# Optimization experiments

Measured on AMD Instinct MI355X. Metric: run time of the kernel, lower is better.

## Reference

```python
import jax, jax.numpy as jnp
import numpy as np
from jax import lax

# dims
B = 1024          # batch
C_IN = 8          # board feature planes
HW = 8            # board side
FN = 16           # filter_num
SEN, INT, OUT = 1024, 2048, 1024
TOT = SEN + INT + OUT            # 4096
CNN_OUT = sum((HW - k + 1) ** 2 for k in range(1, 9)) * FN  # 204*FN = 3264
NUM_OUT = 1968
LORA_R = 64
LORA_SCALE = 128.0 / LORA_R      # alpha / rank = 2.0
TIMESTEPS = 5
DENSITY = 0.3


def setup_inputs() -> dict:
    key = jax.random.key(0)
    ks = jax.random.split(key, 20)
    inp = {"x": jax.random.normal(ks[0], (B, HW, HW, C_IN), dtype=jnp.float32)}
    # conv bank: kernels 1..8, OIHW layout
    for i, k in enumerate(range(1, 9)):
        inp[f"conv_w{k}"] = jax.random.normal(ks[1 + i], (FN, C_IN, k, k), dtype=jnp.float32) * (1.0 / np.sqrt(C_IN * k * k))
    inp["conv_b"] = jnp.zeros((8, FN), dtype=jnp.float32)
    # recurrent weight with sparsity pattern (mask = W != 0, as in register_buffer('sparsity_mask', W_init != 0))
    Wd = jax.random.normal(ks[9], (TOT, TOT), dtype=jnp.float32) * 0.02
    mask = (jax.random.uniform(ks[10], (TOT, TOT)) < DENSITY).astype(jnp.float32)
    inp["W"] = Wd * mask
    inp["lora_A"] = jax.random.normal(ks[11], (TOT, LORA_R), dtype=jnp.float32) * 0.02
    inp["lora_B"] = jax.random.normal(ks[12], (LORA_R, TOT), dtype=jnp.float32) * 0.02
    inp["ip_w"] = jax.random.normal(ks[13], (CNN_OUT, SEN), dtype=jnp.float32) * (1.0 / np.sqrt(CNN_OUT))
    inp["ip_b"] = jnp.zeros((SEN,), dtype=jnp.float32)
    inp["out_w"] = jax.random.normal(ks[14], (OUT, NUM_OUT), dtype=jnp.float32) * (1.0 / np.sqrt(OUT))
    inp["out_b"] = jnp.zeros((NUM_OUT,), dtype=jnp.float32)
    return inp


def _forward(x, conv_w1, conv_w2, conv_w3, conv_w4, conv_w5, conv_w6, conv_w7, conv_w8,
             conv_b, W, lora_A, lora_B, ip_w, ip_b, out_w, out_b):
    xn = jnp.transpose(x, (0, 3, 1, 2))  # NHWC -> NCHW, as x.permute(0,3,1,2)
    feats = []
    for i, cw in enumerate([conv_w1, conv_w2, conv_w3, conv_w4, conv_w5, conv_w6, conv_w7, conv_w8]):
        y = lax.conv_general_dilated(xn, cw, (1, 1), 'VALID',
                                     dimension_numbers=('NCHW', 'OIHW', 'NCHW'))
        y = jax.nn.relu(y + conv_b[i][None, :, None, None])  # use_relu=True
        feats.append(y.reshape(y.shape[0], -1))
    feat = jnp.concatenate(feats, axis=1)  # [B, CNN_OUT]

    # effective W with LoRA + sparsity mask
    mask = (W != 0).astype(W.dtype)
    W_eff = (W + (lora_A @ lora_B) * LORA_SCALE) * mask

    E = feat @ ip_w + ip_b                           # input_proj (no dropout: drop_out=False)
    E_pad = jnp.pad(E, ((0, 0), (0, TOT - SEN)))     # E feeds only the sensory block

    # The nine block matmuls S@Wss + I@Wrs + O@Wos etc. equal slices of state @ W_eff.
    state = jnp.zeros((x.shape[0], TOT), dtype=W.dtype)
    for t in range(TIMESTEPS):
        nxt = state @ W_eff
        if t == 0:
            nxt = nxt + E_pad
        nxt = state + nxt          # use_residual=True
        state = jax.nn.relu(nxt)

    O_state = state[:, SEN + INT:]
    return O_state @ out_w + out_b


def reference(x, conv_w1, conv_w2, conv_w3, conv_w4, conv_w5, conv_w6, conv_w7, conv_w8,
              conv_b, W, lora_A, lora_B, ip_w, ip_b, out_w, out_b):
    return _forward(x, conv_w1, conv_w2, conv_w3, conv_w4, conv_w5, conv_w6, conv_w7, conv_w8,
                    conv_b, W, lora_A, lora_B, ip_w, ip_b, out_w, out_b)
```

## Files before the change

kernel.cpp:

```cpp
#include <hip/hip_runtime.h>
#include <stdint.h>

typedef unsigned short u16;
typedef __attribute__((ext_vector_type(8))) short bf16x8;
typedef __attribute__((ext_vector_type(4))) float f32x4;

__device__ __forceinline__ u16 f2bf(float f) {
  union { float f; uint32_t u; } v; v.f = f;
  uint32_t u = v.u;
  return (u16)((u + 0x7fffu + ((u >> 16) & 1u)) >> 16);
}

__device__ __forceinline__ void gl_lds16(const void* g, void* l) {
  __builtin_amdgcn_global_load_lds(
      (const __attribute__((address_space(1))) uint32_t*)g,
      (__attribute__((address_space(3))) uint32_t*)l, 16, 0, 0);
}

__constant__ int c_off[9] = {0, 1024, 1808, 2384, 2784, 3040, 3184, 3248, 3264};

__global__ __launch_bounds__(256)
void prep_all(const float* __restrict__ x, u16* __restrict__ Xb,
              const float* __restrict__ lA, u16* __restrict__ lAb,
              const float* __restrict__ ip_w, u16* __restrict__ ip_wt,
              const float* __restrict__ out_w, u16* __restrict__ out_wt,
              const float* __restrict__ lB, u16* __restrict__ lBt,
              const float* w1, const float* w2, const float* w3, const float* w4,
              const float* w5, const float* w6, const float* w7, const float* w8,
              const float* __restrict__ cb,
              u16* __restrict__ Wct, float* __restrict__ bias_c) {
  __shared__ float tile[64][65];
  int b = blockIdx.x;
  const int t = threadIdx.x;
  if (b < 512) {
    const int i = b * 256 + t;
    const float4 v = ((const float4*)x)[i];
    ((ushort4*)Xb)[i] = make_ushort4(f2bf(v.x), f2bf(v.y), f2bf(v.z), f2bf(v.w));
    return;
  }
  b -= 512;
  if (b < 256) {
    const int i = b * 256 + t;
    const float4 v = ((const float4*)lA)[i];
    ((ushort4*)lAb)[i] = make_ushort4(f2bf(v.x), f2bf(v.y), f2bf(v.z), f2bf(v.w));
    return;
  }
  b -= 256;
  if (b < 1392) {
    const float* src; u16* dst; int R, C, bx, by;
    if (b < 816)        { src = ip_w;  dst = ip_wt;  R = 3264; C = 1024; bx = b % 16; by = b / 16; }
    else if (b < 1328)  { b -= 816;  src = out_w; dst = out_wt; R = 1024; C = 1968; bx = b % 32; by = b / 32; }
    else                { b -= 1328; src = lB;    dst = lBt;    R = 64;   C = 4096; bx = b;      by = 0; }
    const int rb = by << 6, cbs = bx << 6;
    for (int i = 0; i < 16; ++i) {
      const int idx = t + (i << 8);
      const int r = idx >> 6, c = idx & 63;
      float v = 0.f;
      if (cbs + c < C) v = src[(size_t)(rb + r) * C + cbs + c];
      tile[r][c] = v;
    }
    __syncthreads();
    for (int i = 0; i < 16; ++i) {
      const int idx = t + (i << 8);
      const int c = idx >> 6, r = idx & 63;
      dst[(size_t)(cbs + c) * R + rb + r] = f2bf(tile[r][c]);
    }
    return;
  }
  const int o = b - 1392;
  u16* row = Wct + (size_t)o * 512;
  if (t < 128) *(ushort4*)(row + (t << 2)) = make_ushort4(0, 0, 0, 0);
  if (o >= 3264) {
    if (t == 0) bias_c[o] = 0.f;
    return;
  }
  __syncthreads();
  const float* ws[8] = {w1, w2, w3, w4, w5, w6, w7, w8};
  int kidx = 0;
  while (o >= c_off[kidx + 1]) ++kidx;
  const int ks = kidx + 1;
  const int s  = 8 - kidx;
  const int r  = o - c_off[kidx];
  const int f   = r / (s * s);
  const int rem = r - f * s * s;
  const int oi  = rem / s;
  const int oj  = rem - oi * s;
  const float* w = ws[kidx] + (size_t)f * 8 * ks * ks;
  const int ne = 8 * ks * ks;
  for (int e = t; e < ne; e += 256) {
    const int c  = e / (ks * ks);
    const int er = e - c * ks * ks;
    const int di = er / ks;
    const int dj = er - di * ks;
    row[((oi + di) * 8 + (oj + dj)) * 8 + c] = f2bf(w[(c * ks + di) * ks + dj]);
  }
  if (t == 0) bias_c[o] = cb[kidx * 16 + f];
}

__global__ __launch_bounds__(256)
void weff2(const float* __restrict__ W, const u16* __restrict__ lBt,
           const u16* __restrict__ lAb, u16* __restrict__ Wt) {
  __shared__ __align__(16) u16 As_[64 * 64];
  __shared__ __align__(16) u16 Bs_[64 * 64];
  __shared__ __align__(16) float Wl[64 * 64];
  __shared__ u16 Ct[64 * 68];
  const int t = threadIdx.x;
  const int w = t >> 6, lane = t & 63;
  const int nb = blockIdx.x << 6, kb = blockIdx.y << 6;
  const int m0 = (w & 1) << 5, n0 = (w >> 1) << 5;
  const int lr = lane & 15, lq = lane >> 4;

  for (int i = 0; i < 2; ++i) {
    const int c   = (w << 7) + (i << 6) + lane;
    const int row = c >> 3;
    const int kg  = (c & 7) ^ (row & 7);
    gl_lds16(lBt + (size_t)(nb + row) * 64 + (kg << 3), (char*)As_ + c * 16);
    gl_lds16(lAb + (size_t)(kb + row) * 64 + (kg << 3), (char*)Bs_ + c * 16);
  }
  for (int i = 0; i < 4; ++i) {
    const int c   = (w << 8) + (i << 6) + lane;
    const int row = c >> 4;
    const int cc  = (c & 15) ^ (row & 15);
    gl_lds16(W + (size_t)(kb + row) * 4096 + nb + (cc << 2), (char*)Wl + c * 16);
  }
  __syncthreads();

  f32x4 acc[2][2] = {};
  for (int kk = 0; kk < 2; ++kk) {
    const int kg = (kk << 2) + lq;
    const int sw = (kg ^ (lr & 7)) << 3;
    bf16x8 af[2], bf[2];
    for (int i = 0; i < 2; ++i)
      af[i] = *(const bf16x8*)&As_[(m0 + (i << 4) + lr) * 64 + sw];
    for (int j = 0; j < 2; ++j)
      bf[j] = *(const bf16x8*)&Bs_[(n0 + (j << 4) + lr) * 64 + sw];
    for (int i = 0; i < 2; ++i)
      for (int j = 0; j < 2; ++j)
        acc[i][j] = __builtin_amdgcn_mfma_f32_16x16x32_bf16(af[i], bf[j], acc[i][j], 0, 0, 0);
  }

  for (int i = 0; i < 2; ++i) {
    for (int j = 0; j < 2; ++j) {
      const int cg  = n0 + (j << 4) + lr;
      const int rg0 = m0 + (i << 4) + (lq << 2);
      const int ch  = (rg0 >> 2) ^ (cg & 15);
      const float4 wv4 = *(const float4*)&Wl[cg * 64 + (ch << 2)];
      const float wv[4] = {wv4.x, wv4.y, wv4.z, wv4.w};
      for (int r = 0; r < 4; ++r)
        Ct[(rg0 + r) * 68 + cg] =
            (wv[r] != 0.f) ? f2bf(wv[r] + 2.0f * acc[i][j][r]) : (u16)0;
    }
  }
  __syncthreads();

  const int row = t >> 2, kp = (t & 3) << 4;
  u16* dst = Wt + (size_t)(nb + row) * 4096 + kb + kp;
  const u16* src = &Ct[row * 68 + kp];
  for (int i = 0; i < 4; ++i)
    *(ushort4*)(dst + (i << 2)) = *(const ushort4*)(src + (i << 2));
}

template<int EPI, int NR>
__global__ __launch_bounds__(256)
void gemm3b(const u16* __restrict__ A, int lda,
            const u16* __restrict__ Bt, int ldb, int K,
            const float* __restrict__ bias,
            const float* __restrict__ st_in, int st_ld,
            float* __restrict__ outf, int outf_ld,
            u16* __restrict__ outb, int outb_ld, int nvalid) {
  constexpr int BN = NR * 32;
  __shared__ __align__(16) u16 As[3][64 * 64];
  __shared__ __align__(16) u16 Bs[3][BN * 64];
  const int t = threadIdx.x;
  const int w = t >> 6, lane = t & 63;
  const int mb = blockIdx.y << 6, nb = blockIdx.x * BN;
  const int m0 = (w & 1) << 5, n0 = (w >> 1) * (NR << 4);
  const int lr = lane & 15, lq = lane >> 4;

  f32x4 acc[2][NR] = {};
  const int nk = K >> 6;

  auto stage = [&](int kt, int buf) {
    const int kb = kt << 6;
#pragma unroll
    for (int i = 0; i < 2; ++i) {
      const int c   = (w << 7) + (i << 6) + lane;
      const int row = c >> 3;
      const int kg  = (c & 7) ^ (row & 7);
      gl_lds16(A + (size_t)(mb + row) * lda + kb + (kg << 3),
               (char*)As[buf] + c * 16);
    }
#pragma unroll
    for (int i = 0; i < NR; ++i) {
      const int c   = w * (NR * 64) + (i << 6) + lane;
      const int row = c >> 3;
      const int kg  = (c & 7) ^ (row & 7);
      gl_lds16(Bt + (size_t)(nb + row) * ldb + kb + (kg << 3),
               (char*)Bs[buf] + c * 16);
    }
  };

  stage(0, 0);
  stage(1, 1);
  for (int kt = 0; kt < nk; ++kt) {
    const int buf = kt % 3;
    if (kt + 1 < nk) {
      if constexpr (NR == 4) asm volatile("s_waitcnt vmcnt(6)" ::: "memory");
      else                   asm volatile("s_waitcnt vmcnt(4)" ::: "memory");
    } else {
      asm volatile("s_waitcnt vmcnt(0)" ::: "memory");
    }
    __builtin_amdgcn_s_barrier();
    asm volatile("" ::: "memory");
    __builtin_amdgcn_sched_barrier(0);
    if (kt + 2 < nk) stage(kt + 2, (kt + 2) % 3);
    __builtin_amdgcn_s_setprio(1);
#pragma unroll
    for (int kk = 0; kk < 2; ++kk) {
      const int kg = (kk << 2) + lq;
      const int sw = (kg ^ (lr & 7)) << 3;
      bf16x8 af[2], bf[NR];
#pragma unroll
      for (int i = 0; i < 2; ++i)
        af[i] = *(const bf16x8*)&As[buf][(m0 + (i << 4) + lr) * 64 + sw];
#pragma unroll
      for (int j = 0; j < NR; ++j)
        bf[j] = *(const bf16x8*)&Bs[buf][(n0 + (j << 4) + lr) * 64 + sw];
#pragma unroll
      for (int i = 0; i < 2; ++i)
#pragma unroll
        for (int j = 0; j < NR; ++j)
          acc[i][j] = __builtin_amdgcn_mfma_f32_16x16x32_bf16(af[i], bf[j], acc[i][j], 0, 0, 0);
    }
    __builtin_amdgcn_s_setprio(0);
  }

#pragma unroll
  for (int i = 0; i < 2; ++i) {
#pragma unroll
    for (int j = 0; j < NR; ++j) {
      const int cg = nb + n0 + (j << 4) + lr;
#pragma unroll
      for (int r = 0; r < 4; ++r) {
        const int rg = mb + m0 + (i << 4) + (lq << 2) + r;
        float v = acc[i][j][r];
        if (EPI == 1) {
          v += st_in[(size_t)rg * st_ld + cg];
          v = v > 0.f ? v : 0.f;
          outf[(size_t)rg * outf_ld + cg] = v;
          outb[(size_t)rg * outb_ld + cg] = f2bf(v);
        } else if (EPI == 2) {
          if (cg < nvalid)
            outf[(size_t)rg * outf_ld + cg] = v + bias[cg];
        } else {
          v += bias[cg];
          v = v > 0.f ? v : 0.f;
          outb[(size_t)rg * outb_ld + cg] = f2bf(v);
        }
      }
    }
  }
}

__global__ __launch_bounds__(256)
void gemm_e3b(const u16* __restrict__ A, const u16* __restrict__ Bt,
              float* __restrict__ part) {
  __shared__ __align__(16) u16 As[3][64 * 64];
  __shared__ __align__(16) u16 Bs[3][128 * 64];
  const int t = threadIdx.x;
  const int w = t >> 6, lane = t & 63;
  const int mb = blockIdx.y << 6, nb = blockIdx.x << 7;
  const int m0 = (w & 1) << 5, n0 = (w >> 1) << 6;
  const int lr = lane & 15, lq = lane >> 4;
  const int z = blockIdx.z;
  const int k0 = z * 832;
  const int nk = (z == 3) ? 12 : 13;

  f32x4 acc[2][4] = {};

  auto stage = [&](int kt, int buf) {
    const int kb = k0 + (kt << 6);
#pragma unroll
    for (int i = 0; i < 2; ++i) {
      const int c   = (w << 7) + (i << 6) + lane;
      const int row = c >> 3;
      const int kg  = (c & 7) ^ (row & 7);
      gl_lds16(A + (size_t)(mb + row) * 3328 + kb + (kg << 3),
               (char*)As[buf] + c * 16);
    }
#pragma unroll
    for (int i = 0; i < 4; ++i) {
      const int c   = (w << 8) + (i << 6) + lane;
      const int row = c >> 3;
      const int kg  = (c & 7) ^ (row & 7);
      gl_lds16(Bt + (size_t)(nb + row) * 3264 + kb + (kg << 3),
               (char*)Bs[buf] + c * 16);
    }
  };

  stage(0, 0);
  stage(1, 1);
  for (int kt = 0; kt < nk; ++kt) {
    const int buf = kt % 3;
    if (kt + 1 < nk) asm volatile("s_waitcnt vmcnt(6)" ::: "memory");
    else             asm volatile("s_waitcnt vmcnt(0)" ::: "memory");
    __builtin_amdgcn_s_barrier();
    asm volatile("" ::: "memory");
    __builtin_amdgcn_sched_barrier(0);
    if (kt + 2 < nk) stage(kt + 2, (kt + 2) % 3);
    __builtin_amdgcn_s_setprio(1);
#pragma unroll
    for (int kk = 0; kk < 2; ++kk) {
      const int kg = (kk << 2) + lq;
      const int sw = (kg ^ (lr & 7)) << 3;
      bf16x8 af[2], bf[4];
#pragma unroll
      for (int i = 0; i < 2; ++i)
        af[i] = *(const bf16x8*)&As[buf][(m0 + (i << 4) + lr) * 64 + sw];
#pragma unroll
      for (int j = 0; j < 4; ++j)
        bf[j] = *(const bf16x8*)&Bs[buf][(n0 + (j << 4) + lr) * 64 + sw];
#pragma unroll
      for (int i = 0; i < 2; ++i)
#pragma unroll
        for (int j = 0; j < 4; ++j)
          acc[i][j] = __builtin_amdgcn_mfma_f32_16x16x32_bf16(af[i], bf[j], acc[i][j], 0, 0, 0);
    }
    __builtin_amdgcn_s_setprio(0);
  }

  float* dst = part + (size_t)z * 1024 * 1024;
#pragma unroll
  for (int i = 0; i < 2; ++i)
#pragma unroll
    for (int j = 0; j < 4; ++j) {
      const int cg = nb + n0 + (j << 4) + lr;
#pragma unroll
      for (int r = 0; r < 4; ++r) {
        const int rg = mb + m0 + (i << 4) + (lq << 2) + r;
        dst[(size_t)rg * 1024 + cg] = acc[i][j][r];
      }
    }
}

__global__ __launch_bounds__(256)
void e_combine(const float* __restrict__ part, const float* __restrict__ bias,
               float* __restrict__ st_f, u16* __restrict__ st_b) {
  const int i = (blockIdx.x * 256 + threadIdx.x) << 2;
  const int row = i >> 12, col = i & 4095;
  if (col < 1024) {
    const int pi = (row << 10) + col;
    const float4 a = *(const float4*)&part[pi];
    const float4 b = *(const float4*)&part[1024 * 1024 + pi];
    const float4 c = *(const float4*)&part[2 * 1024 * 1024 + pi];
    const float4 d = *(const float4*)&part[3 * 1024 * 1024 + pi];
    const float4 bs = *(const float4*)&bias[col];
    float v[4] = {a.x + b.x + c.x + d.x + bs.x, a.y + b.y + c.y + d.y + bs.y,
                  a.z + b.z + c.z + d.z + bs.z, a.w + b.w + c.w + d.w + bs.w};
    u16 o[4];
    for (int r = 0; r < 4; ++r) {
      v[r] = v[r] > 0.f ? v[r] : 0.f;
      o[r] = f2bf(v[r]);
    }
    *(float4*)&st_f[i] = make_float4(v[0], v[1], v[2], v[3]);
    *(ushort4*)&st_b[i] = make_ushort4(o[0], o[1], o[2], o[3]);
  } else {
    *(float4*)&st_f[i] = make_float4(0.f, 0.f, 0.f, 0.f);
    *(ushort4*)&st_b[i] = make_ushort4(0, 0, 0, 0);
  }
}

extern "C" void kernel_launch(void* const* d_in, const int* in_sizes, int n_in,
                              void* d_out, int out_size, void* d_ws, size_t ws_size,
                              hipStream_t stream) {
  const float* x     = (const float*)d_in[0];
  const float* cw[8];
  for (int i = 0; i < 8; ++i) cw[i] = (const float*)d_in[1 + i];
  const float* convb = (const float*)d_in[9];
  const float* W     = (const float*)d_in[10];
  const float* lA    = (const float*)d_in[11];
  const float* lB    = (const float*)d_in[12];
  const float* ip_w  = (const float*)d_in[13];
  const float* ip_b  = (const float*)d_in[14];
  const float* out_w = (const float*)d_in[15];
  const float* out_b = (const float*)d_in[16];
  float* out = (float*)d_out;

  char* p = (char*)d_ws;
  u16* feat   = (u16*)p;  p += (size_t)1024 * 3328 * 2;
  u16* ip_wt  = (u16*)p;  p += (size_t)1024 * 3264 * 2;
  u16* out_wt = (u16*)p;  p += (size_t)2048 * 1024 * 2;
  u16* Wt     = (u16*)p;  p += (size_t)4096 * 4096 * 2;
  float* st_f[2];
  st_f[0] = (float*)p;    p += (size_t)1024 * 4096 * 4;
  st_f[1] = (float*)p;    p += (size_t)1024 * 4096 * 4;
  u16* st_b[2];
  st_b[0] = (u16*)p;      p += (size_t)1024 * 4096 * 2;
  st_b[1] = (u16*)p;      p += (size_t)1024 * 4096 * 2;

  char* q = (char*)st_f[1];
  u16* Xb       = (u16*)q;  q += (size_t)1024 * 512 * 2;
  u16* Wct      = (u16*)q;  q += (size_t)3328 * 512 * 2;
  float* bias_c = (float*)q; q += (size_t)3328 * 4;
  u16* lBt      = (u16*)q;  q += (size_t)4096 * 64 * 2;
  u16* lAb      = (u16*)q;  q += (size_t)4096 * 64 * 2;
  float* Epart  = (float*)st_f[1];

  prep_all<<<5488, 256, 0, stream>>>(x, Xb, lA, lAb, ip_w, ip_wt,
                                     out_w, out_wt, lB, lBt,
                                     cw[0], cw[1], cw[2], cw[3],
                                     cw[4], cw[5], cw[6], cw[7], convb,
                                     Wct, bias_c);

  weff2<<<dim3(64, 64), 256, 0, stream>>>(W, lBt, lAb, Wt);

  gemm3b<3, 4><<<dim3(26, 16), 256, 0, stream>>>(Xb, 512, Wct, 512, 512,
      bias_c, nullptr, 0, nullptr, 0, feat, 3328, 3328);

  gemm_e3b<<<dim3(8, 16, 4), 256, 0, stream>>>(feat, ip_wt, Epart);
  e_combine<<<4096, 256, 0, stream>>>(Epart, ip_b, st_f[0], st_b[0]);

  gemm3b<1, 4><<<dim3(32, 16), 256, 0, stream>>>(st_b[0], 4096, Wt, 4096, 1024,
      nullptr, st_f[0], 4096, st_f[1], 4096, st_b[1], 4096, 4096);

  gemm3b<1, 4><<<dim3(32, 16), 256, 0, stream>>>(st_b[1], 4096, Wt, 4096, 4096,
      nullptr, st_f[1], 4096, st_f[0], 4096, st_b[0], 4096, 4096);
  gemm3b<1, 4><<<dim3(32, 16), 256, 0, stream>>>(st_b[0], 4096, Wt, 4096, 4096,
      nullptr, st_f[0], 4096, st_f[1], 4096, st_b[1], 4096, 4096);

  gemm3b<1, 2><<<dim3(16, 16), 256, 0, stream>>>(st_b[1], 4096,
      Wt + (size_t)3072 * 4096, 4096, 4096,
      nullptr, st_f[1] + 3072, 4096, st_f[0] + 3072, 4096,
      st_b[0] + 3072, 4096, 4096);

  gemm3b<2, 2><<<dim3(32, 16), 256, 0, stream>>>(st_b[0] + 3072, 4096, out_wt, 1024, 1024,
      out_b, nullptr, 0, out, 1968, nullptr, 0, 1968);
}
```

Baseline: 393.6 us.

## Load A fragments directly into registers instead of staging through LDS

Both GEMM kernels drop the A-tile LDS staging and instead have each lane load its A fragments straight from global memory into registers, double-buffered one k-step ahead. The loop is manually unrolled by two so the register buffers ping-pong, and the vmcnt waits are adjusted for the extra outstanding loads. This removes A's LDS traffic and footprint, but A rows are now read redundantly by the two wave columns and with less coalesced access, and register pressure goes up.

```diff
diff --git a/kernel.cpp b/kernel.cpp
--- a/kernel.cpp
+++ b/kernel.cpp
@@ -169,7 +169,6 @@
             float* __restrict__ outf, int outf_ld,
             u16* __restrict__ outb, int outb_ld, int nvalid) {
   constexpr int BN = NR * 32;
-  __shared__ __align__(16) u16 As[3][64 * 64];
   __shared__ __align__(16) u16 Bs[3][BN * 64];
   const int t = threadIdx.x;
   const int w = t >> 6, lane = t & 63;
@@ -180,16 +179,19 @@
   f32x4 acc[2][NR] = {};
   const int nk = K >> 6;
 
-  auto stage = [&](int kt, int buf) {
+  const u16* Abase = A + (size_t)(mb + m0 + lr) * lda + (lq << 3);
+
+  auto loadA = [&](bf16x8 (&af)[2][2], int kt) {
     const int kb = kt << 6;
 #pragma unroll
-    for (int i = 0; i < 2; ++i) {
-      const int c   = (w << 7) + (i << 6) + lane;
-      const int row = c >> 3;
-      const int kg  = (c & 7) ^ (row & 7);
-      gl_lds16(A + (size_t)(mb + row) * lda + kb + (kg << 3),
-               (char*)As[buf] + c * 16);
-    }
+    for (int i = 0; i < 2; ++i)
+#pragma unroll
+      for (int kk = 0; kk < 2; ++kk)
+        af[i][kk] = *(const bf16x8*)(Abase + (size_t)(i << 4) * lda + kb + (kk << 5));
+  };
+
+  auto stageB = [&](int kt, int buf) {
+    const int kb = kt << 6;
 #pragma unroll
     for (int i = 0; i < NR; ++i) {
       const int c   = w * (NR * 64) + (i << 6) + lane;
@@ -200,29 +202,25 @@
     }
   };
 
-  stage(0, 0);
-  stage(1, 1);
-  for (int kt = 0; kt < nk; ++kt) {
+  auto iter = [&](int kt, bf16x8 (&afc)[2][2], bf16x8 (&afn)[2][2]) {
     const int buf = kt % 3;
     if (kt + 1 < nk) {
-      if constexpr (NR == 4) asm volatile("s_waitcnt vmcnt(6)" ::: "memory");
-      else                   asm volatile("s_waitcnt vmcnt(4)" ::: "memory");
+      loadA(afn, kt + 1);
+      if constexpr (NR == 4) asm volatile("s_waitcnt vmcnt(8)" ::: "memory");
+      else                   asm volatile("s_waitcnt vmcnt(6)" ::: "memory");
     } else {
       asm volatile("s_waitcnt vmcnt(0)" ::: "memory");
     }
     __builtin_amdgcn_s_barrier();
     asm volatile("" ::: "memory");
     __builtin_amdgcn_sched_barrier(0);
-    if (kt + 2 < nk) stage(kt + 2, (kt + 2) % 3);
+    if (kt + 2 < nk) stageB(kt + 2, (kt + 2) % 3);
     __builtin_amdgcn_s_setprio(1);
 #pragma unroll
     for (int kk = 0; kk < 2; ++kk) {
       const int kg = (kk << 2) + lq;
       const int sw = (kg ^ (lr & 7)) << 3;
-      bf16x8 af[2], bf[NR];
-#pragma unroll
-      for (int i = 0; i < 2; ++i)
-        af[i] = *(const bf16x8*)&As[buf][(m0 + (i << 4) + lr) * 64 + sw];
+      bf16x8 bf[NR];
 #pragma unroll
       for (int j = 0; j < NR; ++j)
         bf[j] = *(const bf16x8*)&Bs[buf][(n0 + (j << 4) + lr) * 64 + sw];
@@ -230,10 +228,21 @@
       for (int i = 0; i < 2; ++i)
 #pragma unroll
         for (int j = 0; j < NR; ++j)
-          acc[i][j] = __builtin_amdgcn_mfma_f32_16x16x32_bf16(af[i], bf[j], acc[i][j], 0, 0, 0);
+          acc[i][j] = __builtin_amdgcn_mfma_f32_16x16x32_bf16(afc[i][kk], bf[j], acc[i][j], 0, 0, 0);
     }
     __builtin_amdgcn_s_setprio(0);
-  }
+  };
+
+  bf16x8 afA[2][2], afB[2][2];
+  loadA(afA, 0);
+  stageB(0, 0);
+  stageB(1, 1);
+  int kt = 0;
+  for (; kt + 1 < nk; kt += 2) {
+    iter(kt, afA, afB);
+    iter(kt + 1, afB, afA);
+  }
+  if (kt < nk) iter(kt, afA, afB);
 
 #pragma unroll
   for (int i = 0; i < 2; ++i) {
@@ -265,7 +274,6 @@
 __global__ __launch_bounds__(256)
 void gemm_e3b(const u16* __restrict__ A, const u16* __restrict__ Bt,
               float* __restrict__ part) {
-  __shared__ __align__(16) u16 As[3][64 * 64];
   __shared__ __align__(16) u16 Bs[3][128 * 64];
   const int t = threadIdx.x;
   const int w = t >> 6, lane = t & 63;
@@ -278,16 +286,19 @@
 
   f32x4 acc[2][4] = {};
 
-  auto stage = [&](int kt, int buf) {
+  const u16* Abase = A + (size_t)(mb + m0 + lr) * 3328 + k0 + (lq << 3);
+
+  auto loadA = [&](bf16x8 (&af)[2][2], int kt) {
+    const int kb = kt << 6;
+#pragma unroll
+    for (int i = 0; i < 2; ++i)
+#pragma unroll
+      for (int kk = 0; kk < 2; ++kk)
+        af[i][kk] = *(const bf16x8*)(Abase + (size_t)(i << 4) * 3328 + kb + (kk << 5));
+  };
+
+  auto stageB = [&](int kt, int buf) {
     const int kb = k0 + (kt << 6);
-#pragma unroll
-    for (int i = 0; i < 2; ++i) {
-      const int c   = (w << 7) + (i << 6) + lane;
-      const int row = c >> 3;
-      const int kg  = (c & 7) ^ (row & 7);
-      gl_lds16(A + (size_t)(mb + row) * 3328 + kb + (kg << 3),
-               (char*)As[buf] + c * 16);
-    }
 #pragma unroll
     for (int i = 0; i < 4; ++i) {
       const int c   = (w << 8) + (i << 6) + lane;
@@ -298,25 +309,24 @@
     }
   };
 
-  stage(0, 0);
-  stage(1, 1);
-  for (int kt = 0; kt < nk; ++kt) {
+  auto iter = [&](int kt, bf16x8 (&afc)[2][2], bf16x8 (&afn)[2][2]) {
     const int buf = kt % 3;
-    if (kt + 1 < nk) asm volatile("s_waitcnt vmcnt(6)" ::: "memory");
-    else             asm volatile("s_waitcnt vmcnt(0)" ::: "memory");
+    if (kt + 1 < nk) {
+      loadA(afn, kt + 1);
+      asm volatile("s_waitcnt vmcnt(8)" ::: "memory");
+    } else {
+      asm volatile("s_waitcnt vmcnt(0)" ::: "memory");
+    }
     __builtin_amdgcn_s_barrier();
     asm volatile("" ::: "memory");
     __builtin_amdgcn_sched_barrier(0);
-    if (kt + 2 < nk) stage(kt + 2, (kt + 2) % 3);
+    if (kt + 2 < nk) stageB(kt + 2, (kt + 2) % 3);
     __builtin_amdgcn_s_setprio(1);
 #pragma unroll
     for (int kk = 0; kk < 2; ++kk) {
       const int kg = (kk << 2) + lq;
       const int sw = (kg ^ (lr & 7)) << 3;
-      bf16x8 af[2], bf[4];
-#pragma unroll
-      for (int i = 0; i < 2; ++i)
-        af[i] = *(const bf16x8*)&As[buf][(m0 + (i << 4) + lr) * 64 + sw];
+      bf16x8 bf[4];
 #pragma unroll
       for (int j = 0; j < 4; ++j)
         bf[j] = *(const bf16x8*)&Bs[buf][(n0 + (j << 4) + lr) * 64 + sw];
@@ -324,10 +334,21 @@
       for (int i = 0; i < 2; ++i)
 #pragma unroll
         for (int j = 0; j < 4; ++j)
-          acc[i][j] = __builtin_amdgcn_mfma_f32_16x16x32_bf16(af[i], bf[j], acc[i][j], 0, 0, 0);
+          acc[i][j] = __builtin_amdgcn_mfma_f32_16x16x32_bf16(afc[i][kk], bf[j], acc[i][j], 0, 0, 0);
     }
     __builtin_amdgcn_s_setprio(0);
-  }
+  };
+
+  bf16x8 afA[2][2], afB[2][2];
+  loadA(afA, 0);
+  stageB(0, 0);
+  stageB(1, 1);
+  int kt = 0;
+  for (; kt + 1 < nk; kt += 2) {
+    iter(kt, afA, afB);
+    iter(kt + 1, afB, afA);
+  }
+  if (kt < nk) iter(kt, afA, afB);
 
   float* dst = part + (size_t)z * 1024 * 1024;
 #pragma unroll
```

Result: slower. 460.1 us (+16.9%).
